# Kernel optimization log

Measured on AMD Instinct MI355X. Metric: run time of the kernel, lower is better.

## Reference

```python
import jax, jax.numpy as jnp
import numpy as np

# Module constants (from init_kwargs / derived)
KH, KW = 3, 3
STRIDE = (1, 1)
PAD = (1, 1)
DIL = (1, 1)
N_OFFSET_GRPS = 8  # offset.shape[1] // (2*KH*KW) = 144 // 18
N_WEIGHT_GRPS = 1


def setup_inputs() -> dict:
    key = jax.random.key(0)
    k1, k2, k3, k4, k5 = jax.random.split(key, 5)
    B, C, H, W = 4, 64, 128, 128
    inp = {
        "input": jax.random.normal(k1, (B, C, H, W), dtype=jnp.float32),
        "offset": jax.random.normal(k2, (B, 2 * N_OFFSET_GRPS * KH * KW, H, W), dtype=jnp.float32),
        "mask": jax.random.uniform(k3, (B, N_OFFSET_GRPS * KH * KW, H, W), dtype=jnp.float32),
        "weight": jax.random.normal(k4, (64, C, KH, KW), dtype=jnp.float32) * 0.05,
        "bias": jax.random.normal(k5, (64,), dtype=jnp.float32) * 0.05,
    }
    return inp


def _deform_conv2d(x, offset, mask, weight, bias):
    B, C, H, W = x.shape
    Ho, Wo = offset.shape[2], offset.shape[3]
    G = N_OFFSET_GRPS
    K = KH * KW
    Cg = C // G

    # base (un-deformed) sampling positions per kernel tap and output pixel
    ky, kx = jnp.meshgrid(jnp.arange(KH), jnp.arange(KW), indexing="ij")
    ky = ky.reshape(K)
    kx = kx.reshape(K)
    oy = jnp.arange(Ho) * STRIDE[0] - PAD[0]
    ox = jnp.arange(Wo) * STRIDE[1] - PAD[1]
    base_y = (oy[None, :, None] + (ky * DIL[0])[:, None, None]).astype(x.dtype)  # [K,Ho,1]
    base_x = (ox[None, None, :] + (kx * DIL[1])[:, None, None]).astype(x.dtype)  # [K,1,Wo]

    off = offset.reshape(B, G, K, 2, Ho, Wo)  # [...,0]=dy, [...,1]=dx
    py = base_y[None, None] + off[:, :, :, 0]  # [B,G,K,Ho,Wo]
    px = base_x[None, None] + off[:, :, :, 1]

    y0 = jnp.floor(py)
    x0 = jnp.floor(px)
    ly = py - y0  # fractional parts
    lx = px - x0
    y0i = y0.astype(jnp.int32)
    x0i = x0.astype(jnp.int32)

    xg = x.reshape(B, G, Cg, H * W)  # per-offset-group channel slices

    def corner(yi, xi):
        valid = ((yi >= 0) & (yi < H) & (xi >= 0) & (xi < W)).astype(x.dtype)
        idx = jnp.clip(yi, 0, H - 1) * W + jnp.clip(xi, 0, W - 1)  # [B,G,K,Ho,Wo]
        gather = lambda xbg, ibg: xbg[:, ibg]  # [Cg,H*W],[K,Ho,Wo] -> [Cg,K,Ho,Wo]
        v = jax.vmap(jax.vmap(gather))(xg, idx)  # [B,G,Cg,K,Ho,Wo]
        return v * valid[:, :, None]

    w00 = (1 - ly) * (1 - lx)
    w01 = (1 - ly) * lx
    w10 = ly * (1 - lx)
    w11 = ly * lx
    samp = (corner(y0i, x0i) * w00[:, :, None]
            + corner(y0i, x0i + 1) * w01[:, :, None]
            + corner(y0i + 1, x0i) * w10[:, :, None]
            + corner(y0i + 1, x0i + 1) * w11[:, :, None])  # [B,G,Cg,K,Ho,Wo]

    samp = samp * mask.reshape(B, G, 1, K, Ho, Wo)  # DCNv2 modulation
    col = samp.reshape(B, C, K, Ho, Wo)
    wr = weight.reshape(weight.shape[0], C, K)  # groups == 1
    out = jnp.einsum("ock,bckhw->bohw", wr, col) + bias[None, :, None, None]
    return out


def reference(input, offset, mask, weight, bias):
    return _deform_conv2d(input, offset, mask, weight, bias)
```

## Files before the change

### kernel.cpp

```cpp
#include <hip/hip_runtime.h>

#define HH 128
#define WW 128
#define CC 64
#define CO 64
#define BB 4
#define GG 8
#define CG 8
#define KK 9
#define HW (HH*WW)

typedef __attribute__((ext_vector_type(8))) short short8;
typedef __attribute__((ext_vector_type(4))) float floatx4;
typedef __attribute__((ext_vector_type(2))) float f32x2;

union S8I { short8 s; int i[4]; };
union FU { float f; unsigned u; };

__device__ inline short f2bf(float f) {
    FU v; v.f = f;
    return (short)((v.u + 0x7FFF + ((v.u >> 16) & 1)) >> 16);
}
__device__ inline unsigned rnd2(float f) {
    FU v; v.f = f;
    return v.u + 0x8000u;
}
__device__ inline float bflo(int e) { union { int i; float f; } u; u.i = e << 16; return u.f; }
__device__ inline float bfhi(int e) { union { int i; float f; } u; u.i = e & 0xffff0000; return u.f; }

__global__ __launch_bounds__(256)
void prep(const float* __restrict__ wt, const float* __restrict__ in,
          short* __restrict__ wf, short* __restrict__ in_t) {
    const int bid = blockIdx.x;
    if (bid < 144) {
        const int tid = bid * 256 + threadIdx.x;
        const int j   = tid & 7;
        const int L   = (tid >> 3) & 63;
        const int fid = tid >> 9;
        const int ot  = fid & 3;
        const int gch = fid >> 2;
        const int h   = gch / 9, gc = gch - h * 9;
        const int o   = ot * 16 + (L & 15);
        const int g   = h * 4 + (L >> 4);
        wf[tid] = f2bf(wt[o * 576 + (g * 8 + j) * 9 + gc]);
    } else {
        const int idx = bid - 144;
        const int bx = idx & 63;
        const int g  = (idx >> 6) & 7;
        const int b  = idx >> 9;
        const int p  = bx * 256 + threadIdx.x;
        const float* src = in + (b * CC + g * CG) * HW + p;
        short8 v;
        #pragma unroll
        for (int cg = 0; cg < CG; ++cg) v[cg] = f2bf(src[cg * HW]);
        *(short8*)(in_t + ((b * GG + g) * HW + p) * 8) = v;
    }
}

__global__ __launch_bounds__(256, 4)
void dcn_fused(const short* __restrict__ in_t, const float* __restrict__ off,
               const float* __restrict__ msk, const short* __restrict__ wf,
               const float* __restrict__ bias, float* __restrict__ out)
{
    __shared__ short s_wf[36 * 512];

    const int t = threadIdx.x;

    const int lin = (blockIdx.x & 7) * 128 + (blockIdx.x >> 3);
    const int b   = lin >> 8;
    const int rem = lin & 255;
    const int ho  = rem >> 1;
    const int bx  = rem & 1;

    const int w = t >> 6, lane = t & 63;
    const int q4 = lane >> 4, n16 = lane & 15;
    const int px = bx * 64 + w * 16 + n16;
    const int basepix = ho * WW + px;

    floatx4 acc[4];
    #pragma unroll
    for (int ot = 0; ot < 4; ++ot)
        #pragma unroll
        for (int r = 0; r < 4; ++r)
            acc[ot][r] = bias[ot * 16 + q4 * 4 + r];

    const char* ib = (const char*)(in_t + (long)b * GG * HW * 8);

    #pragma unroll
    for (int h = 0; h < 2; ++h) {
        if (h) __syncthreads();
        #pragma unroll
        for (int k = 0; k < 9; ++k) {
            const int idx = (k * 256 + t) * 8;
            *(short8*)(s_wf + idx) = *(const short8*)(wf + h * 18432 + idx);
        }
        __syncthreads();

        const int g = h * 4 + q4;

        float pdy[9], pdx[9], pm[9];
        #pragma unroll
        for (int i = 0; i < 9; ++i) {
            const int offc = (b * 144 + g * 18 + i * 2) * HW + basepix;
            pdy[i] = off[offc];
            pdx[i] = off[offc + HW];
            pm[i]  = msk[(b * 72 + g * 9 + i) * HW + basepix];
        }

        const int gsh = g << 18;

        #pragma unroll
        for (int q = 0; q < 3; ++q) {
            const int i0 = q * 3;
            S8I u00[3], u01[3], u10[3], u11[3];
            float cw00[3], cw01[3], cw10[3], cw11[3];

            #pragma unroll
            for (int j = 0; j < 3; ++j) {
                const int i = i0 + j;
                const int ky = i / 3, kx = i - (i / 3) * 3;

                const float py  = (float)(ho - 1 + ky) + pdy[i];
                const float pxf = (float)(px - 1 + kx) + pdx[i];
                const float y0f = floorf(py), x0f = floorf(pxf);
                const float ly = py - y0f, lx = pxf - x0f;
                const int y0 = (int)y0f, x0 = (int)x0f;
                const int y1 = y0 + 1,  x1 = x0 + 1;

                const float vy0 = (y0 >= 0 && y0 < HH) ? 1.f : 0.f;
                const float vy1 = (y1 >= 0 && y1 < HH) ? 1.f : 0.f;
                const float vx0 = (x0 >= 0 && x0 < WW) ? 1.f : 0.f;
                const float vx1 = (x1 >= 0 && x1 < WW) ? 1.f : 0.f;
                const int y0c = min(max(y0, 0), HH - 1), y1c = min(max(y1, 0), HH - 1);
                const int x0c = min(max(x0, 0), WW - 1), x1c = min(max(x1, 0), WW - 1);

                const float m = pm[i];
                const float wy0 = (1.f - ly) * vy0 * m;
                const float wy1 = ly * vy1 * m;
                const float wx0 = (1.f - lx) * vx0;
                const float wx1 = lx * vx1;
                cw00[j] = wy0 * wx0; cw01[j] = wy0 * wx1;
                cw10[j] = wy1 * wx0; cw11[j] = wy1 * wx1;

                const int y0sh = gsh + (y0c << 11), y1sh = gsh + (y1c << 11);
                const int x0sh = x0c << 4, x1sh = x1c << 4;
                u00[j].s = *(const short8*)(ib + (y0sh + x0sh));
                u01[j].s = *(const short8*)(ib + (y0sh + x1sh));
                u10[j].s = *(const short8*)(ib + (y1sh + x0sh));
                u11[j].s = *(const short8*)(ib + (y1sh + x1sh));
            }

            __builtin_amdgcn_sched_barrier(0);

            #pragma unroll
            for (int j = 0; j < 3; ++j) {
                const int i = i0 + j;
                const f32x2 W00 = {cw00[j], cw00[j]}, W01 = {cw01[j], cw01[j]};
                const f32x2 W10 = {cw10[j], cw10[j]}, W11 = {cw11[j], cw11[j]};
                S8I res;
                #pragma unroll
                for (int pc = 0; pc < 4; ++pc) {
                    const int e00 = u00[j].i[pc], e01 = u01[j].i[pc];
                    const int e10 = u10[j].i[pc], e11 = u11[j].i[pc];
                    f32x2 a00 = {bflo(e00), bfhi(e00)};
                    f32x2 a01 = {bflo(e01), bfhi(e01)};
                    f32x2 a10 = {bflo(e10), bfhi(e10)};
                    f32x2 a11 = {bflo(e11), bfhi(e11)};
                    f32x2 v = a00 * W00;
                    v += a01 * W01;
                    v += a10 * W10;
                    v += a11 * W11;
                    res.i[pc] = (int)__builtin_amdgcn_perm(rnd2(v.y), rnd2(v.x), 0x07060302u);
                }

                #pragma unroll
                for (int ot = 0; ot < 4; ++ot) {
                    const short8 afr = *(const short8*)&s_wf[(i * 4 + ot) * 512 + lane * 8];
                    acc[ot] = __builtin_amdgcn_mfma_f32_16x16x32_bf16(afr, res.s, acc[ot], 0, 0, 0);
                }
            }
        }
    }

    #pragma unroll
    for (int ot = 0; ot < 4; ++ot)
        #pragma unroll
        for (int r = 0; r < 4; ++r)
            out[((b * CO + ot * 16 + q4 * 4 + r) * HH + ho) * WW + px] = acc[ot][r];
}

extern "C" void kernel_launch(void* const* d_in, const int* in_sizes, int n_in,
                              void* d_out, int out_size, void* d_ws, size_t ws_size,
                              hipStream_t stream) {
    const float* in   = (const float*)d_in[0];
    const float* off  = (const float*)d_in[1];
    const float* msk  = (const float*)d_in[2];
    const float* wt   = (const float*)d_in[3];
    const float* bias = (const float*)d_in[4];
    float* out = (float*)d_out;
    short* wf   = (short*)d_ws;
    short* in_t = (short*)d_ws + 36864;

    prep<<<144 + 2048, 256, 0, stream>>>(wt, in, wf, in_t);

    dcn_fused<<<1024, 256, 0, stream>>>(in_t, off, msk, wf, bias, out);
}
```

Baseline: 135.0 us.

## Stage input halo tile in LDS for bilinear gathers, read weights from global

```diff
diff --git a/kernel.cpp b/kernel.cpp
--- a/kernel.cpp
+++ b/kernel.cpp
@@ -9,6 +9,9 @@
 #define CG 8
 #define KK 9
 #define HW (HH*WW)
+
+#define TROWS 13
+#define TPX   33
 
 typedef __attribute__((ext_vector_type(8))) short short8;
 typedef __attribute__((ext_vector_type(4))) float floatx4;
@@ -58,24 +61,30 @@
 }
 
 __global__ __launch_bounds__(256, 4)
-void dcn_fused(const short* __restrict__ in_t, const float* __restrict__ off,
-               const float* __restrict__ msk, const short* __restrict__ wf,
-               const float* __restrict__ bias, float* __restrict__ out)
+void dcn_tile(const short* __restrict__ in_t, const float* __restrict__ off,
+              const float* __restrict__ msk, const short* __restrict__ wf,
+              const float* __restrict__ bias, float* __restrict__ out)
 {
-    __shared__ short s_wf[36 * 512];
+    __shared__ short tile[4 * TROWS * TPX * 8];
 
     const int t = threadIdx.x;
 
     const int lin = (blockIdx.x & 7) * 128 + (blockIdx.x >> 3);
     const int b   = lin >> 8;
     const int rem = lin & 255;
-    const int ho  = rem >> 1;
-    const int bx  = rem & 1;
+    const int rq  = rem >> 3;
+    const int pxg = rem & 7;
+    const int rb  = rq << 2;
+    const int pxbase = pxg << 4;
 
     const int w = t >> 6, lane = t & 63;
     const int q4 = lane >> 4, n16 = lane & 15;
-    const int px = bx * 64 + w * 16 + n16;
-    const int basepix = ho * WW + px;
+    const int row = rb + w;
+    const int px  = pxbase + n16;
+    const int basepix = row * WW + px;
+
+    const int ylo = rb - 4;
+    const int xlo = pxbase - 8;
 
     floatx4 acc[4];
     #pragma unroll
@@ -90,13 +99,24 @@
     for (int h = 0; h < 2; ++h) {
         if (h) __syncthreads();
         #pragma unroll
-        for (int k = 0; k < 9; ++k) {
-            const int idx = (k * 256 + t) * 8;
-            *(short8*)(s_wf + idx) = *(const short8*)(wf + h * 18432 + idx);
+        for (int it = 0; it < 7; ++it) {
+            const int s = it * 256 + t;
+            if (s < 4 * TROWS * TPX) {
+                const int gl = s / (TROWS * TPX);
+                const int r2 = s - gl * (TROWS * TPX);
+                const int rs = r2 / TPX;
+                const int xs = r2 - rs * TPX;
+                const int y  = min(max(ylo + rs, 0), HH - 1);
+                const int x  = min(max(xlo + xs, 0), WW - 1);
+                const int g  = h * 4 + gl;
+                const short8 v = *(const short8*)(ib + (g << 18) + (y << 11) + (x << 4));
+                *(short8*)(tile + ((gl * TROWS + rs) * TPX + xs) * 8) = v;
+            }
         }
         __syncthreads();
 
-        const int g = h * 4 + q4;
+        const int g   = h * 4 + q4;
+        const int gsh = g << 18;
 
         float pdy[9], pdx[9], pm[9];
         #pragma unroll
@@ -107,8 +127,6 @@
             pm[i]  = msk[(b * 72 + g * 9 + i) * HW + basepix];
         }
 
-        const int gsh = g << 18;
-
         #pragma unroll
         for (int q = 0; q < 3; ++q) {
             const int i0 = q * 3;
@@ -120,7 +138,7 @@
                 const int i = i0 + j;
                 const int ky = i / 3, kx = i - (i / 3) * 3;
 
-                const float py  = (float)(ho - 1 + ky) + pdy[i];
+                const float py  = (float)(row - 1 + ky) + pdy[i];
                 const float pxf = (float)(px - 1 + kx) + pdx[i];
                 const float y0f = floorf(py), x0f = floorf(pxf);
                 const float ly = py - y0f, lx = pxf - x0f;
@@ -142,12 +160,31 @@
                 cw00[j] = wy0 * wx0; cw01[j] = wy0 * wx1;
                 cw10[j] = wy1 * wx0; cw11[j] = wy1 * wx1;
 
-                const int y0sh = gsh + (y0c << 11), y1sh = gsh + (y1c << 11);
-                const int x0sh = x0c << 4, x1sh = x1c << 4;
-                u00[j].s = *(const short8*)(ib + (y0sh + x0sh));
-                u01[j].s = *(const short8*)(ib + (y0sh + x1sh));
-                u10[j].s = *(const short8*)(ib + (y1sh + x0sh));
-                u11[j].s = *(const short8*)(ib + (y1sh + x1sh));
+                const int ys0r = y0c - ylo, ys1r = y1c - ylo;
+                const int xs0r = x0c - xlo, xs1r = x1c - xlo;
+                const bool iy0 = (unsigned)ys0r <= (TROWS - 1u);
+                const bool iy1 = (unsigned)ys1r <= (TROWS - 1u);
+                const bool ix0 = (unsigned)xs0r <= (TPX - 1u);
+                const bool ix1 = (unsigned)xs1r <= (TPX - 1u);
+                const int ys0 = min(max(ys0r, 0), TROWS - 1);
+                const int ys1 = min(max(ys1r, 0), TROWS - 1);
+                const int xs0 = min(max(xs0r, 0), TPX - 1);
+                const int xs1 = min(max(xs1r, 0), TPX - 1);
+
+                const int gbase = q4 * (TROWS * TPX);
+                u00[j].s = *(const short8*)(tile + ((gbase + ys0 * TPX + xs0)) * 8);
+                u01[j].s = *(const short8*)(tile + ((gbase + ys0 * TPX + xs1)) * 8);
+                u10[j].s = *(const short8*)(tile + ((gbase + ys1 * TPX + xs0)) * 8);
+                u11[j].s = *(const short8*)(tile + ((gbase + ys1 * TPX + xs1)) * 8);
+
+                if (__builtin_expect(!(iy0 && ix0) && cw00[j] != 0.f, 0))
+                    u00[j].s = *(const short8*)(ib + gsh + (y0c << 11) + (x0c << 4));
+                if (__builtin_expect(!(iy0 && ix1) && cw01[j] != 0.f, 0))
+                    u01[j].s = *(const short8*)(ib + gsh + (y0c << 11) + (x1c << 4));
+                if (__builtin_expect(!(iy1 && ix0) && cw10[j] != 0.f, 0))
+                    u10[j].s = *(const short8*)(ib + gsh + (y1c << 11) + (x0c << 4));
+                if (__builtin_expect(!(iy1 && ix1) && cw11[j] != 0.f, 0))
+                    u11[j].s = *(const short8*)(ib + gsh + (y1c << 11) + (x1c << 4));
             }
 
             __builtin_amdgcn_sched_barrier(0);
@@ -175,7 +212,7 @@
 
                 #pragma unroll
                 for (int ot = 0; ot < 4; ++ot) {
-                    const short8 afr = *(const short8*)&s_wf[(i * 4 + ot) * 512 + lane * 8];
+                    const short8 afr = *(const short8*)&wf[((h * 9 + i) * 4 + ot) * 512 + lane * 8];
                     acc[ot] = __builtin_amdgcn_mfma_f32_16x16x32_bf16(afr, res.s, acc[ot], 0, 0, 0);
                 }
             }
@@ -186,7 +223,7 @@
     for (int ot = 0; ot < 4; ++ot)
         #pragma unroll
         for (int r = 0; r < 4; ++r)
-            out[((b * CO + ot * 16 + q4 * 4 + r) * HH + ho) * WW + px] = acc[ot][r];
+            out[((b * CO + ot * 16 + q4 * 4 + r) * HH + row) * WW + px] = acc[ot][r];
 }
 
 extern "C" void kernel_launch(void* const* d_in, const int* in_sizes, int n_in,
@@ -203,5 +240,5 @@
 
     prep<<<144 + 2048, 256, 0, stream>>>(wt, in, wf, in_t);
 
-    dcn_fused<<<1024, 256, 0, stream>>>(in_t, off, msk, wf, bias, out);
-}
+    dcn_tile<<<1024, 256, 0, stream>>>(in_t, off, msk, wf, bias, out);
+}
```

Result: slower. 138.4 us (+2.5%).

## Issue all 36 gather loads up front with staged vmcnt waits

Applied to the files above, without the earlier changes.

```diff
diff --git a/kernel.cpp b/kernel.cpp
--- a/kernel.cpp
+++ b/kernel.cpp
@@ -27,6 +27,8 @@
 }
 __device__ inline float bflo(int e) { union { int i; float f; } u; u.i = e << 16; return u.f; }
 __device__ inline float bfhi(int e) { union { int i; float f; } u; u.i = e & 0xffff0000; return u.f; }
+
+template<int N> struct Int { static constexpr int value = N; };
 
 __global__ __launch_bounds__(256)
 void prep(const float* __restrict__ wt, const float* __restrict__ in,
@@ -57,10 +59,10 @@
     }
 }
 
-__global__ __launch_bounds__(256, 4)
-void dcn_fused(const short* __restrict__ in_t, const float* __restrict__ off,
-               const float* __restrict__ msk, const short* __restrict__ wf,
-               const float* __restrict__ bias, float* __restrict__ out)
+__global__ __launch_bounds__(256, 2)
+void dcn_mlp(const short* __restrict__ in_t, const float* __restrict__ off,
+             const float* __restrict__ msk, const short* __restrict__ wf,
+             const float* __restrict__ bias, float* __restrict__ out)
 {
     __shared__ short s_wf[36 * 512];
 
@@ -96,7 +98,8 @@
         }
         __syncthreads();
 
-        const int g = h * 4 + q4;
+        const int g   = h * 4 + q4;
+        const int gsh = g << 18;
 
         float pdy[9], pdx[9], pm[9];
         #pragma unroll
@@ -107,79 +110,92 @@
             pm[i]  = msk[(b * 72 + g * 9 + i) * HW + basepix];
         }
 
-        const int gsh = g << 18;
-
-        #pragma unroll
-        for (int q = 0; q < 3; ++q) {
-            const int i0 = q * 3;
-            S8I u00[3], u01[3], u10[3], u11[3];
-            float cw00[3], cw01[3], cw10[3], cw11[3];
-
+        float cw00[9], cw01[9], cw10[9], cw11[9];
+        int o00[9], o01[9], o10[9], o11[9];
+        #pragma unroll
+        for (int i = 0; i < 9; ++i) {
+            const int ky = i / 3, kx = i - (i / 3) * 3;
+
+            const float py  = (float)(ho - 1 + ky) + pdy[i];
+            const float pxf = (float)(px - 1 + kx) + pdx[i];
+            const float y0f = floorf(py), x0f = floorf(pxf);
+            const float ly = py - y0f, lx = pxf - x0f;
+            const int y0 = (int)y0f, x0 = (int)x0f;
+            const int y1 = y0 + 1,  x1 = x0 + 1;
+
+            const float vy0 = (y0 >= 0 && y0 < HH) ? 1.f : 0.f;
+            const float vy1 = (y1 >= 0 && y1 < HH) ? 1.f : 0.f;
+            const float vx0 = (x0 >= 0 && x0 < WW) ? 1.f : 0.f;
+            const float vx1 = (x1 >= 0 && x1 < WW) ? 1.f : 0.f;
+            const int y0c = min(max(y0, 0), HH - 1), y1c = min(max(y1, 0), HH - 1);
+            const int x0c = min(max(x0, 0), WW - 1), x1c = min(max(x1, 0), WW - 1);
+
+            const float m = pm[i];
+            const float wy0 = (1.f - ly) * vy0 * m;
+            const float wy1 = ly * vy1 * m;
+            const float wx0 = (1.f - lx) * vx0;
+            const float wx1 = lx * vx1;
+            cw00[i] = wy0 * wx0; cw01[i] = wy0 * wx1;
+            cw10[i] = wy1 * wx0; cw11[i] = wy1 * wx1;
+
+            const int y0sh = gsh + (y0c << 11), y1sh = gsh + (y1c << 11);
+            const int x0sh = x0c << 4, x1sh = x1c << 4;
+            o00[i] = y0sh + x0sh; o01[i] = y0sh + x1sh;
+            o10[i] = y1sh + x0sh; o11[i] = y1sh + x1sh;
+        }
+
+        S8I u00[9], u01[9], u10[9], u11[9];
+        #pragma unroll
+        for (int i = 0; i < 9; ++i) {
+            asm volatile("global_load_dwordx4 %0, %1, off"
+                         : "=&v"(u00[i].s) : "v"(ib + o00[i]) : "memory");
+            asm volatile("global_load_dwordx4 %0, %1, off"
+                         : "=&v"(u01[i].s) : "v"(ib + o01[i]) : "memory");
+            asm volatile("global_load_dwordx4 %0, %1, off"
+                         : "=&v"(u10[i].s) : "v"(ib + o10[i]) : "memory");
+            asm volatile("global_load_dwordx4 %0, %1, off"
+                         : "=&v"(u11[i].s) : "v"(ib + o11[i]) : "memory");
+        }
+
+        auto consume = [&](auto tag) {
+            constexpr int i  = decltype(tag)::value;
+            constexpr int vm = 4 * (8 - i);
+            asm volatile("s_waitcnt vmcnt(%0)" :: "n"(vm) : "memory");
+            __builtin_amdgcn_sched_barrier(0);
+
+            const f32x2 W00 = {cw00[i], cw00[i]}, W01 = {cw01[i], cw01[i]};
+            const f32x2 W10 = {cw10[i], cw10[i]}, W11 = {cw11[i], cw11[i]};
+            S8I res;
             #pragma unroll
-            for (int j = 0; j < 3; ++j) {
-                const int i = i0 + j;
-                const int ky = i / 3, kx = i - (i / 3) * 3;
-
-                const float py  = (float)(ho - 1 + ky) + pdy[i];
-                const float pxf = (float)(px - 1 + kx) + pdx[i];
-                const float y0f = floorf(py), x0f = floorf(pxf);
-                const float ly = py - y0f, lx = pxf - x0f;
-                const int y0 = (int)y0f, x0 = (int)x0f;
-                const int y1 = y0 + 1,  x1 = x0 + 1;
-
-                const float vy0 = (y0 >= 0 && y0 < HH) ? 1.f : 0.f;
-                const float vy1 = (y1 >= 0 && y1 < HH) ? 1.f : 0.f;
-                const float vx0 = (x0 >= 0 && x0 < WW) ? 1.f : 0.f;
-                const float vx1 = (x1 >= 0 && x1 < WW) ? 1.f : 0.f;
-                const int y0c = min(max(y0, 0), HH - 1), y1c = min(max(y1, 0), HH - 1);
-                const int x0c = min(max(x0, 0), WW - 1), x1c = min(max(x1, 0), WW - 1);
-
-                const float m = pm[i];
-                const float wy0 = (1.f - ly) * vy0 * m;
-                const float wy1 = ly * vy1 * m;
-                const float wx0 = (1.f - lx) * vx0;
-                const float wx1 = lx * vx1;
-                cw00[j] = wy0 * wx0; cw01[j] = wy0 * wx1;
-                cw10[j] = wy1 * wx0; cw11[j] = wy1 * wx1;
-
-                const int y0sh = gsh + (y0c << 11), y1sh = gsh + (y1c << 11);
-                const int x0sh = x0c << 4, x1sh = x1c << 4;
-                u00[j].s = *(const short8*)(ib + (y0sh + x0sh));
-                u01[j].s = *(const short8*)(ib + (y0sh + x1sh));
-                u10[j].s = *(const short8*)(ib + (y1sh + x0sh));
-                u11[j].s = *(const short8*)(ib + (y1sh + x1sh));
+            for (int pc = 0; pc < 4; ++pc) {
+                const int e00 = u00[i].i[pc], e01 = u01[i].i[pc];
+                const int e10 = u10[i].i[pc], e11 = u11[i].i[pc];
+                f32x2 a00 = {bflo(e00), bfhi(e00)};
+                f32x2 a01 = {bflo(e01), bfhi(e01)};
+                f32x2 a10 = {bflo(e10), bfhi(e10)};
+                f32x2 a11 = {bflo(e11), bfhi(e11)};
+                f32x2 v = a00 * W00;
+                v += a01 * W01;
+                v += a10 * W10;
+                v += a11 * W11;
+                res.i[pc] = (int)__builtin_amdgcn_perm(rnd2(v.y), rnd2(v.x), 0x07060302u);
             }
 
-            __builtin_amdgcn_sched_barrier(0);
-
             #pragma unroll
-            for (int j = 0; j < 3; ++j) {
-                const int i = i0 + j;
-                const f32x2 W00 = {cw00[j], cw00[j]}, W01 = {cw01[j], cw01[j]};
-                const f32x2 W10 = {cw10[j], cw10[j]}, W11 = {cw11[j], cw11[j]};
-                S8I res;
-                #pragma unroll
-                for (int pc = 0; pc < 4; ++pc) {
-                    const int e00 = u00[j].i[pc], e01 = u01[j].i[pc];
-                    const int e10 = u10[j].i[pc], e11 = u11[j].i[pc];
-                    f32x2 a00 = {bflo(e00), bfhi(e00)};
-                    f32x2 a01 = {bflo(e01), bfhi(e01)};
-                    f32x2 a10 = {bflo(e10), bfhi(e10)};
-                    f32x2 a11 = {bflo(e11), bfhi(e11)};
-                    f32x2 v = a00 * W00;
-                    v += a01 * W01;
-                    v += a10 * W10;
-                    v += a11 * W11;
-                    res.i[pc] = (int)__builtin_amdgcn_perm(rnd2(v.y), rnd2(v.x), 0x07060302u);
-                }
-
-                #pragma unroll
-                for (int ot = 0; ot < 4; ++ot) {
-                    const short8 afr = *(const short8*)&s_wf[(i * 4 + ot) * 512 + lane * 8];
-                    acc[ot] = __builtin_amdgcn_mfma_f32_16x16x32_bf16(afr, res.s, acc[ot], 0, 0, 0);
-                }
+            for (int ot = 0; ot < 4; ++ot) {
+                const short8 afr = *(const short8*)&s_wf[(i * 4 + ot) * 512 + lane * 8];
+                acc[ot] = __builtin_amdgcn_mfma_f32_16x16x32_bf16(afr, res.s, acc[ot], 0, 0, 0);
             }
-        }
+        };
+        consume(Int<0>{});
+        consume(Int<1>{});
+        consume(Int<2>{});
+        consume(Int<3>{});
+        consume(Int<4>{});
+        consume(Int<5>{});
+        consume(Int<6>{});
+        consume(Int<7>{});
+        consume(Int<8>{});
     }
 
     #pragma unroll
@@ -203,5 +219,5 @@
 
     prep<<<144 + 2048, 256, 0, stream>>>(wt, in, wf, in_t);
 
-    dcn_fused<<<1024, 256, 0, stream>>>(in_t, off, msk, wf, bias, out);
-}
+    dcn_mlp<<<1024, 256, 0, stream>>>(in_t, off, msk, wf, bias, out);
+}
```

Measured after the change: 133.7 us. About the same (-1.0%).
